# Kernel tuning notes

Measured on AMD Instinct MI355X. Metric: run time of the kernel, lower is better.

## Reference

```python
import jax, jax.numpy as jnp
import numpy as np

H = 16  # num_attention_heads
LN_EPS = 1e-12


def setup_inputs() -> dict:
    key = jax.random.key(0)
    ks = jax.random.split(key, 13)
    S, B, D = 2048, 2, 1024
    std = 0.02
    return {
        "query_tensor": jax.random.normal(ks[0], (S, B, D), jnp.float32),
        "key_tensor": jax.random.normal(ks[1], (S, B, D), jnp.float32),
        "value_tensor": jax.random.normal(ks[2], (S, B, D), jnp.float32),
        "Wq": jax.random.normal(ks[3], (D, D), jnp.float32) * std,
        "bq": jnp.zeros((D,), jnp.float32),
        "Wk": jax.random.normal(ks[4], (D, D), jnp.float32) * std,
        "bk": jnp.zeros((D,), jnp.float32),
        "Wv": jax.random.normal(ks[5], (D, D), jnp.float32) * std,
        "bv": jnp.zeros((D,), jnp.float32),
        "Wo": jax.random.normal(ks[6], (D, D), jnp.float32) * std,
        "bo": jnp.zeros((D,), jnp.float32),
        "ln_w": jnp.ones((D,), jnp.float32),
        "ln_b": jnp.zeros((D,), jnp.float32),
    }


def _layernorm(x, w, b):
    u = jnp.mean(x, axis=-1, keepdims=True)
    s = jnp.mean(jnp.square(x - u), axis=-1, keepdims=True)
    return w * ((x - u) / jnp.sqrt(s + LN_EPS)) + b


def reference(query_tensor, key_tensor, value_tensor, Wq, bq, Wk, bk, Wv, bv, Wo, bo, ln_w, ln_b):
    S, B, D = query_tensor.shape
    dh = D // H
    # QKV projections (nn.Linear: x @ W.T + b)
    q = query_tensor @ Wq.T + bq          # (S, B, D)
    k = key_tensor @ Wk.T + bk            # (Sk, B, D)
    v = value_tensor @ Wv.T + bv          # (Sk, B, D)
    # (S, B, D) -> (B*H, S, dh)
    q = q.reshape(S, B * H, dh).transpose(1, 0, 2)
    k = k.reshape(-1, B * H, dh).transpose(1, 0, 2)
    v = v.reshape(-1, B * H, dh).transpose(1, 0, 2)
    # NOTE: original code has NO 1/sqrt(dh) scaling
    scores = jnp.einsum('nqd,nkd->nqk', q, k)            # (B*H, S, Sk)
    probs = jax.nn.softmax(scores, axis=-1)
    # dropout is identity in eval mode
    ctx = jnp.einsum('nqk,nkd->nqd', probs, v)           # (B*H, S, dh)
    ctx = ctx.transpose(1, 0, 2).reshape(S, B, D)
    # BertSelfOutput: dense + residual + LayerNorm (dropout identity)
    out = ctx @ Wo.T + bo
    return _layernorm(out + query_tensor, ln_w, ln_b)
```

## Files before the change

### kernel.cpp

```cpp
#include <hip/hip_runtime.h>

#define SEQ    2048
#define BATCH  2
#define DMODEL 1024
#define NHEAD  16
#define DH     64
#define MROWS  (SEQ*BATCH)
#define RS     (BATCH*DMODEL)
#define LN_EPS 1e-12f
#define LOG2E  1.4426950408889634f

typedef __attribute__((ext_vector_type(8))) short short8;
typedef __attribute__((ext_vector_type(4))) float floatx4;

#define AS_GLOBAL __attribute__((address_space(1)))
#define AS_LDS    __attribute__((address_space(3)))

__device__ __forceinline__ float bf2f(unsigned short s) {
    union { unsigned u; float f; } a; a.u = ((unsigned)s) << 16; return a.f;
}
__device__ __forceinline__ unsigned short f2bf(float x) {
    union { float f; unsigned u; } a; a.f = x;
    unsigned r = a.u + 0x7fffu + ((a.u >> 16) & 1u);
    return (unsigned short)(r >> 16);
}
__device__ __forceinline__ unsigned cvt_pk_bf16(float a, float b) {
    unsigned r;
    asm("v_cvt_pk_bf16_f32 %0, %1, %2" : "=v"(r) : "v"(a), "v"(b));
    return r;
}
__device__ __forceinline__ float max3f(float a, float b, float c) {
    float r;
    asm("v_max3_f32 %0, %1, %2, %3" : "=v"(r) : "v"(a), "v"(b), "v"(c));
    return r;
}
__device__ __forceinline__ float fast_exp2(float x) {
#if __has_builtin(__builtin_amdgcn_exp2f)
    return __builtin_amdgcn_exp2f(x);
#else
    return exp2f(x);
#endif
}
__device__ __forceinline__ uint4 cvt8(const float* __restrict__ p) {
    float4 x0 = *(const float4*)(p);
    float4 x1 = *(const float4*)(p + 4);
    union { uint4 u; unsigned short s[8]; } r;
    r.s[0] = f2bf(x0.x); r.s[1] = f2bf(x0.y);
    r.s[2] = f2bf(x0.z); r.s[3] = f2bf(x0.w);
    r.s[4] = f2bf(x1.x); r.s[5] = f2bf(x1.y);
    r.s[6] = f2bf(x1.z); r.s[7] = f2bf(x1.w);
    return r.u;
}
__device__ __forceinline__ uint4 cvt8s(const float* __restrict__ p, float sc) {
    float4 x0 = *(const float4*)(p);
    float4 x1 = *(const float4*)(p + 4);
    union { uint4 u; unsigned short s[8]; } r;
    r.s[0] = f2bf(x0.x*sc); r.s[1] = f2bf(x0.y*sc);
    r.s[2] = f2bf(x0.z*sc); r.s[3] = f2bf(x0.w*sc);
    r.s[4] = f2bf(x1.x*sc); r.s[5] = f2bf(x1.y*sc);
    r.s[6] = f2bf(x1.z*sc); r.s[7] = f2bf(x1.w*sc);
    return r.u;
}

__global__ void beacon_kernel(float* out, float val) {
    if (threadIdx.x == 0) out[0] = val;
}

__global__ __launch_bounds__(256)
void cvt_kernel(const float* __restrict__ s0, const float* __restrict__ s1,
                const float* __restrict__ s2, const float* __restrict__ s3,
                const float* __restrict__ s4, const float* __restrict__ s5,
                const float* __restrict__ s6,
                unsigned short* __restrict__ d0, unsigned short* __restrict__ d1,
                unsigned short* __restrict__ d2, unsigned short* __restrict__ d3,
                unsigned short* __restrict__ d4, unsigned short* __restrict__ d5,
                unsigned short* __restrict__ d6)
{
    const float* srcs[7] = {s0, s1, s2, s3, s4, s5, s6};
    unsigned short* dsts[7] = {d0, d1, d2, d3, d4, d5, d6};
    const int cnts[7] = {4194304, 4194304, 4194304, 1048576, 1048576, 1048576, 1048576};
    const float scl[7] = {1.f, 1.f, 1.f, LOG2E, 1.f, 1.f, 1.f};
    const int z = blockIdx.z;
    const float* src = srcs[z];
    unsigned short* dst = dsts[z];
    const int count = cnts[z];
    const float sc = scl[z];
    const int stride = gridDim.x * 256 * 8;
    for (int i = (blockIdx.x * 256 + threadIdx.x) * 8; i < count; i += stride)
        *(uint4*)&dst[i] = cvt8s(&src[i], sc);
}

__global__ __launch_bounds__(256)
void vt_kernel(const unsigned short* __restrict__ Vb,
               unsigned short* __restrict__ VT)
{
    __shared__ __align__(16) short T[64*72];
    const int tid = threadIdx.x;
    const int s0 = blockIdx.x * 64;
    const int bh = blockIdx.y;
    const int b = bh >> 4, h = bh & 15;

    #pragma unroll
    for (int rep = 0; rep < 2; ++rep) {
        int c = tid + rep * 256;
        int s = c >> 3, cc = c & 7;
        *(uint4*)&T[s*72 + cc*8] =
            *(const uint4*)&Vb[((s0 + s) * BATCH + b) * DMODEL + h*64 + cc*8];
    }
    __syncthreads();
    #pragma unroll
    for (int rep = 0; rep < 2; ++rep) {
        int o = tid + rep * 256;
        int d = o >> 3, sc = o & 7;
        union { uint4 u; unsigned short e[8]; } pk;
        #pragma unroll
        for (int j = 0; j < 8; ++j)
            pk.e[j] = (unsigned short)T[(sc*8 + j)*72 + d];
        *(uint4*)&VT[bh*(DH*SEQ) + d*SEQ + s0 + sc*8] = pk.u;
    }
}

template<int OUTF32>
__device__ __forceinline__ void gemm_bf16_body(
    const unsigned short* __restrict__ A,
    const unsigned short* __restrict__ W,
    const float* __restrict__ bias, float bscale,
    void* __restrict__ Cout)
{
    __shared__ __align__(16) short Alds[2][128*32];
    __shared__ __align__(16) short Blds[2][128*32];

    const int tid  = threadIdx.x;
    const int lane = tid & 63;
    const int wave = tid >> 6;
    const int lrow = lane & 15;
    const int lq   = lane >> 4;
    const int m0 = blockIdx.x * 128;
    const int n0 = blockIdx.y * 128;
    const int mw = (wave >> 1) * 64;
    const int nw = (wave & 1) * 64;
    const int K  = DMODEL;

    const int chunk0 = tid;
    const int chunk1 = tid + 256;
    const int row0 = chunk0 >> 2, col0 = (chunk0 & 3) << 3;
    const int row1 = chunk1 >> 2, col1 = (chunk1 & 3) << 3;
    const unsigned short* gA0 = &A[(m0 + row0) * K + col0];
    const unsigned short* gA1 = &A[(m0 + row1) * K + col1];
    const unsigned short* gB0 = &W[(n0 + row0) * K + col0];
    const unsigned short* gB1 = &W[(n0 + row1) * K + col1];

    auto stage = [&](int k0, int b) {
        __builtin_amdgcn_global_load_lds((const AS_GLOBAL unsigned int*)(gA0 + k0),
            (AS_LDS unsigned int*)&Alds[b][(wave*64)*8], 16, 0, 0);
        __builtin_amdgcn_global_load_lds((const AS_GLOBAL unsigned int*)(gA1 + k0),
            (AS_LDS unsigned int*)&Alds[b][(256 + wave*64)*8], 16, 0, 0);
        __builtin_amdgcn_global_load_lds((const AS_GLOBAL unsigned int*)(gB0 + k0),
            (AS_LDS unsigned int*)&Blds[b][(wave*64)*8], 16, 0, 0);
        __builtin_amdgcn_global_load_lds((const AS_GLOBAL unsigned int*)(gB1 + k0),
            (AS_LDS unsigned int*)&Blds[b][(256 + wave*64)*8], 16, 0, 0);
    };

    floatx4 zero = {0.f, 0.f, 0.f, 0.f};
    floatx4 acc[4][4];
    #pragma unroll
    for (int i = 0; i < 4; ++i)
        #pragma unroll
        for (int j = 0; j < 4; ++j) acc[i][j] = zero;

    stage(0, 0);
    __syncthreads();

    for (int k0 = 0; k0 < K; k0 += 32) {
        const int cur = (k0 >> 5) & 1;
        if (k0 + 32 < K) stage(k0 + 32, cur ^ 1);
        short8 af[4], bfg[4];
        #pragma unroll
        for (int mi = 0; mi < 4; ++mi)
            af[mi] = *(const short8*)&Alds[cur][(mw + mi*16 + lrow)*32 + lq*8];
        #pragma unroll
        for (int ni = 0; ni < 4; ++ni)
            bfg[ni] = *(const short8*)&Blds[cur][(nw + ni*16 + lrow)*32 + lq*8];
        #pragma unroll
        for (int mi = 0; mi < 4; ++mi)
            #pragma unroll
            for (int ni = 0; ni < 4; ++ni)
                acc[mi][ni] = __builtin_amdgcn_mfma_f32_16x16x32_bf16(af[mi], bfg[ni], acc[mi][ni], 0, 0, 0);
        __syncthreads();
    }

    #pragma unroll
    for (int mi = 0; mi < 4; ++mi) {
        #pragma unroll
        for (int ni = 0; ni < 4; ++ni) {
            int n = n0 + nw + ni*16 + lrow;
            float bv_ = bias[n] * bscale;
            #pragma unroll
            for (int r = 0; r < 4; ++r) {
                int m = m0 + mw + mi*16 + lq*4 + r;
                float v = acc[mi][ni][r] + bv_;
                if (OUTF32) ((float*)Cout)[m * DMODEL + n] = v;
                else ((unsigned short*)Cout)[m * DMODEL + n] = f2bf(v);
            }
        }
    }
}

__global__ __launch_bounds__(256)
void qkv_bf16(const unsigned short* __restrict__ qb, const unsigned short* __restrict__ kb,
              const unsigned short* __restrict__ vb,
              const unsigned short* __restrict__ Wqb, const float* __restrict__ bq,
              const unsigned short* __restrict__ Wkb, const float* __restrict__ bk,
              const unsigned short* __restrict__ Wvb, const float* __restrict__ bv,
              unsigned short* __restrict__ Qo, unsigned short* __restrict__ Ko,
              unsigned short* __restrict__ Vo)
{
    const unsigned short *A, *W; const float* B; unsigned short* C; float bs;
    if (blockIdx.z == 0)      { A = qb; W = Wqb; B = bq; C = Qo; bs = LOG2E; }
    else if (blockIdx.z == 1) { A = kb; W = Wkb; B = bk; C = Ko; bs = 1.f; }
    else                      { A = vb; W = Wvb; B = bv; C = Vo; bs = 1.f; }
    gemm_bf16_body<0>(A, W, B, bs, C);
}

__global__ __launch_bounds__(256)
void oproj_bf16(const unsigned short* __restrict__ Cx,
                const unsigned short* __restrict__ Wob, const float* __restrict__ bo,
                float* __restrict__ O32)
{
    gemm_bf16_body<1>(Cx, Wob, bo, 1.f, O32);
}

__global__ __launch_bounds__(256)
void qkv_mfma(const float* __restrict__ q_in, const float* __restrict__ k_in,
              const float* __restrict__ v_in,
              const float* __restrict__ Wq, const float* __restrict__ bq,
              const float* __restrict__ Wk, const float* __restrict__ bk,
              const float* __restrict__ Wv, const float* __restrict__ bv,
              unsigned short* __restrict__ Qo, unsigned short* __restrict__ Ko,
              unsigned short* __restrict__ Vo)
{
    const float *A, *W, *B; unsigned short* C;
    if (blockIdx.z == 0)      { A = q_in; W = Wq; B = bq; C = Qo; }
    else if (blockIdx.z == 1) { A = k_in; W = Wk; B = bk; C = Ko; }
    else                      { A = v_in; W = Wv; B = bv; C = Vo; }

    __shared__ __align__(16) short Alds[128*32];
    __shared__ __align__(16) short Blds[128*32];
    const int tid  = threadIdx.x;
    const int lane = tid & 63;
    const int wave = tid >> 6;
    const int lrow = lane & 15;
    const int lq   = lane >> 4;
    const int m0 = blockIdx.x * 128;
    const int n0 = blockIdx.y * 128;
    const int mw = (wave >> 1) * 64;
    const int nw = (wave & 1) * 64;
    const int K  = DMODEL;

    floatx4 zero = {0.f, 0.f, 0.f, 0.f};
    floatx4 acc[4][4];
    #pragma unroll
    for (int i = 0; i < 4; ++i)
        #pragma unroll
        for (int j = 0; j < 4; ++j) acc[i][j] = zero;

    for (int k0 = 0; k0 < K; k0 += 32) {
        #pragma unroll
        for (int rep = 0; rep < 2; ++rep) {
            int chunk = tid + rep * 256;
            int row = chunk >> 2;
            int col = (chunk & 3) << 3;
            *(uint4*)&Alds[row*32 + col] = cvt8(&A[(m0 + row) * K + k0 + col]);
            *(uint4*)&Blds[row*32 + col] = cvt8(&W[(n0 + row) * K + k0 + col]);
        }
        __syncthreads();
        short8 af[4], bfg[4];
        #pragma unroll
        for (int mi = 0; mi < 4; ++mi)
            af[mi] = *(const short8*)&Alds[(mw + mi*16 + lrow)*32 + lq*8];
        #pragma unroll
        for (int ni = 0; ni < 4; ++ni)
            bfg[ni] = *(const short8*)&Blds[(nw + ni*16 + lrow)*32 + lq*8];
        #pragma unroll
        for (int mi = 0; mi < 4; ++mi)
            #pragma unroll
            for (int ni = 0; ni < 4; ++ni)
                acc[mi][ni] = __builtin_amdgcn_mfma_f32_16x16x32_bf16(af[mi], bfg[ni], acc[mi][ni], 0, 0, 0);
        __syncthreads();
    }

    #pragma unroll
    for (int mi = 0; mi < 4; ++mi) {
        #pragma unroll
        for (int ni = 0; ni < 4; ++ni) {
            int n = n0 + nw + ni*16 + lrow;
            float bv_ = B[n];
            #pragma unroll
            for (int r = 0; r < 4; ++r) {
                int m = m0 + mw + mi*16 + lq*4 + r;
                C[m * DMODEL + n] = f2bf(acc[mi][ni][r] + bv_);
            }
        }
    }
}

__global__ __launch_bounds__(256)
void oproj_mfma(const unsigned short* __restrict__ Cx,
                const float* __restrict__ Wo, const float* __restrict__ bo,
                float* __restrict__ O32)
{
    __shared__ __align__(16) short Alds[128*32];
    __shared__ __align__(16) short Blds[128*32];
    const int tid  = threadIdx.x;
    const int lane = tid & 63;
    const int wave = tid >> 6;
    const int lrow = lane & 15;
    const int lq   = lane >> 4;
    const int m0 = blockIdx.x * 128;
    const int n0 = blockIdx.y * 128;
    const int mw = (wave >> 1) * 64;
    const int nw = (wave & 1) * 64;
    const int K  = DMODEL;

    floatx4 zero = {0.f, 0.f, 0.f, 0.f};
    floatx4 acc[4][4];
    #pragma unroll
    for (int i = 0; i < 4; ++i)
        #pragma unroll
        for (int j = 0; j < 4; ++j) acc[i][j] = zero;

    for (int k0 = 0; k0 < K; k0 += 32) {
        #pragma unroll
        for (int rep = 0; rep < 2; ++rep) {
            int chunk = tid + rep * 256;
            int row = chunk >> 2;
            int col = (chunk & 3) << 3;
            *(uint4*)&Alds[row*32 + col] = *(const uint4*)&Cx[(m0 + row) * K + k0 + col];
            *(uint4*)&Blds[row*32 + col] = cvt8(&Wo[(n0 + row) * K + k0 + col]);
        }
        __syncthreads();
        short8 af[4], bfg[4];
        #pragma unroll
        for (int mi = 0; mi < 4; ++mi)
            af[mi] = *(const short8*)&Alds[(mw + mi*16 + lrow)*32 + lq*8];
        #pragma unroll
        for (int ni = 0; ni < 4; ++ni)
            bfg[ni] = *(const short8*)&Blds[(nw + ni*16 + lrow)*32 + lq*8];
        #pragma unroll
        for (int mi = 0; mi < 4; ++mi)
            #pragma unroll
            for (int ni = 0; ni < 4; ++ni)
                acc[mi][ni] = __builtin_amdgcn_mfma_f32_16x16x32_bf16(af[mi], bfg[ni], acc[mi][ni], 0, 0, 0);
        __syncthreads();
    }

    #pragma unroll
    for (int mi = 0; mi < 4; ++mi) {
        #pragma unroll
        for (int ni = 0; ni < 4; ++ni) {
            int n = n0 + nw + ni*16 + lrow;
            float bv_ = bo[n];
            #pragma unroll
            for (int r = 0; r < 4; ++r) {
                int m = m0 + mw + mi*16 + lq*4 + r;
                O32[m * DMODEL + n] = acc[mi][ni][r] + bv_;
            }
        }
    }
}

__global__ __launch_bounds__(256)
void attn_mfma5(const unsigned short* __restrict__ Q,
                const unsigned short* __restrict__ Kg,
                const unsigned short* __restrict__ VT,
                unsigned short* __restrict__ Ctx)
{
    __shared__ __align__(16) short SMEM[20480];

    const int tid  = threadIdx.x;
    const int lane = tid & 63;
    const int wave = tid >> 6;
    const int lrow = lane & 15;
    const int lq   = lane >> 4;

    const int q0 = blockIdx.x * 64;
    const int bh = blockIdx.y;
    const int off = (bh >> 4) * DMODEL + (bh & 15) * DH;
    const unsigned short* VTb = VT + bh * (DH * SEQ);
    short* const psw = &SMEM[16384 + wave * 1024];

    auto stageKV = [&](int kt, int b) {
        const int kbase = kt * 64;
        short* ksb = &SMEM[b * 8192];
        short* vtb = &SMEM[b * 8192 + 4096];
        #pragma unroll
        for (int rep = 0; rep < 2; ++rep) {
            int c = rep*256 + tid;
            int r = c >> 3, cc = c & 7;
            int sw = ((cc ^ (r & 7)) << 3);
            __builtin_amdgcn_global_load_lds(
                (const AS_GLOBAL unsigned int*)&Kg[(kbase + r) * RS + off + sw],
                (AS_LDS unsigned int*)&ksb[(rep*256 + wave*64) * 8], 16, 0, 0);
            __builtin_amdgcn_global_load_lds(
                (const AS_GLOBAL unsigned int*)&VTb[r * SEQ + kbase + sw],
                (AS_LDS unsigned int*)&vtb[(rep*256 + wave*64) * 8], 16, 0, 0);
        }
    };

    stageKV(0, 0);

    const int qrow = q0 + wave*16 + lrow;
    short8 qf[2];
    qf[0] = *(const short8*)&Q[qrow * RS + off + lq*8];
    qf[1] = *(const short8*)&Q[qrow * RS + off + 32 + lq*8];

    floatx4 zero = {0.f, 0.f, 0.f, 0.f};
    float m_i = 0.f, l_i = 0.f;
    floatx4 oacc[4];
    #pragma unroll
    for (int ni = 0; ni < 4; ++ni) oacc[ni] = zero;

    __syncthreads();

    for (int kt = 0; kt < SEQ/64; ++kt) {
        const int cur = kt & 1;
        if (kt + 1 < SEQ/64) stageKV(kt + 1, cur ^ 1);
        const short* ksb = &SMEM[cur * 8192];
        const short* vtb = &SMEM[cur * 8192 + 4096];

        floatx4 sacc[4];
        const float negm = -m_i;
        floatx4 minit = {negm, negm, negm, negm};
        #pragma unroll
        for (int ni = 0; ni < 4; ++ni) sacc[ni] = minit;
        __builtin_amdgcn_s_setprio(1);
        #pragma unroll
        for (int ni = 0; ni < 4; ++ni) {
            #pragma unroll
            for (int kk = 0; kk < 2; ++kk) {
                int key = ni*16 + lrow;
                int cc  = kk*4 + lq;
                short8 kf = *(const short8*)&ksb[key*64 + ((cc ^ (key & 7)) << 3)];
                sacc[ni] = __builtin_amdgcn_mfma_f32_16x16x32_bf16(kf, qf[kk], sacc[ni], 0, 0, 0);
            }
        }
        __builtin_amdgcn_s_setprio(0);

        float a0 = max3f(sacc[0][0], sacc[0][1], sacc[0][2]);
        float a1 = max3f(sacc[0][3], sacc[1][0], sacc[1][1]);
        float a2 = max3f(sacc[1][2], sacc[1][3], sacc[2][0]);
        float a3 = max3f(sacc[2][1], sacc[2][2], sacc[2][3]);
        float a4 = max3f(sacc[3][0], sacc[3][1], sacc[3][2]);
        float b0 = max3f(a0, a1, a2);
        float b1 = max3f(a3, a4, sacc[3][3]);
        float mx = fmaxf(b0, b1);
        mx = fmaxf(mx, __shfl_xor(mx, 16));
        mx = fmaxf(mx, __shfl_xor(mx, 32));

        float p[4][4];
        if (__all(mx <= 8.f)) {
            #pragma unroll
            for (int ni = 0; ni < 4; ++ni)
                #pragma unroll
                for (int r = 0; r < 4; ++r)
                    p[ni][r] = fast_exp2(sacc[ni][r]);
        } else {
            float shift = fmaxf(mx, 0.f);
            float alpha = fast_exp2(-shift);
            l_i *= alpha;
            #pragma unroll
            for (int ni = 0; ni < 4; ++ni)
                #pragma unroll
                for (int r = 0; r < 4; ++r) oacc[ni][r] *= alpha;
            m_i += shift;
            #pragma unroll
            for (int ni = 0; ni < 4; ++ni)
                #pragma unroll
                for (int r = 0; r < 4; ++r)
                    p[ni][r] = fast_exp2(sacc[ni][r] - shift);
        }

        float s00 = (p[0][0] + p[0][1]) + (p[0][2] + p[0][3]);
        float s01 = (p[1][0] + p[1][1]) + (p[1][2] + p[1][3]);
        float s10 = (p[2][0] + p[2][1]) + (p[2][2] + p[2][3]);
        float s11 = (p[3][0] + p[3][1]) + (p[3][2] + p[3][3]);
        float psum = (s00 + s01) + (s10 + s11);
        psum += __shfl_xor(psum, 16);
        psum += __shfl_xor(psum, 32);
        l_i += psum;

        #pragma unroll
        for (int ni = 0; ni < 4; ++ni) {
            uint2 pk;
            pk.x = cvt_pk_bf16(p[ni][0], p[ni][1]);
            pk.y = cvt_pk_bf16(p[ni][2], p[ni][3]);
            int t  = ni*2 + (lq >> 1);
            int tp = t ^ (lrow & 7);
            *(uint2*)&psw[lrow*64 + tp*8 + (lq & 1)*4] = pk;
        }
        __builtin_amdgcn_wave_barrier();

        short8 pf[2];
        #pragma unroll
        for (int kk = 0; kk < 2; ++kk) {
            int t  = kk*4 + lq;
            int tp = t ^ (lrow & 7);
            pf[kk] = *(const short8*)&psw[lrow*64 + tp*8];
        }

        __builtin_amdgcn_s_setprio(1);
        #pragma unroll
        for (int ni = 0; ni < 4; ++ni) {
            #pragma unroll
            for (int kk = 0; kk < 2; ++kk) {
                int d  = ni*16 + lrow;
                int cc = kk*4 + lq;
                short8 vf = *(const short8*)&vtb[d*64 + ((cc ^ (d & 7)) << 3)];
                oacc[ni] = __builtin_amdgcn_mfma_f32_16x16x32_bf16(vf, pf[kk], oacc[ni], 0, 0, 0);
            }
        }
        __builtin_amdgcn_s_setprio(0);

        __syncthreads();
    }

    const float inv = 1.f / l_i;
    #pragma unroll
    for (int ni = 0; ni < 4; ++ni) {
        uint2 ok;
        ok.x = cvt_pk_bf16(oacc[ni][0] * inv, oacc[ni][1] * inv);
        ok.y = cvt_pk_bf16(oacc[ni][2] * inv, oacc[ni][3] * inv);
        *(uint2*)&Ctx[qrow * RS + off + ni*16 + lq*4] = ok;
    }
}

__global__ __launch_bounds__(256)
void attn_mfma2(const unsigned short* __restrict__ Q,
                const unsigned short* __restrict__ Kg,
                const unsigned short* __restrict__ V,
                unsigned short* __restrict__ Ctx)
{
    __shared__ __align__(16) short Qs[64*72];
    __shared__ __align__(16) short Ks[64*72];
    __shared__ __align__(16) short Vt[64*72];
    __shared__ __align__(16) short Ps[4][16*72];

    const int tid  = threadIdx.x;
    const int lane = tid & 63;
    const int wave = tid >> 6;
    const int lrow = lane & 15;
    const int lq   = lane >> 4;

    const int q0 = blockIdx.x * 64;
    const int bh = blockIdx.y;
    const int off = (bh >> 4) * DMODEL + (bh & 15) * DH;

    #pragma unroll
    for (int rep = 0; rep < 2; ++rep) {
        int chunk = tid + rep * 256;
        int r = chunk >> 3;
        int c = (chunk & 7) << 3;
        *(uint4*)&Qs[r*72 + c] = *(const uint4*)&Q[(q0 + r) * RS + off + c];
    }
    __syncthreads();

    short8 qf[2];
    #pragma unroll
    for (int ks = 0; ks < 2; ++ks)
        qf[ks] = *(const short8*)&Qs[(wave*16 + lrow)*72 + ks*32 + lq*8];

    floatx4 zero = {0.f, 0.f, 0.f, 0.f};
    float m_i = -1e30f, l_i = 0.f;
    floatx4 oacc[4];
    #pragma unroll
    for (int ni = 0; ni < 4; ++ni) oacc[ni] = zero;

    for (int kt = 0; kt < SEQ/64; ++kt) {
        __syncthreads();
        const int kbase = kt * 64;
        #pragma unroll
        for (int rep = 0; rep < 2; ++rep) {
            int chunk = tid + rep * 256;
            int r = chunk >> 3;
            int c = (chunk & 7) << 3;
            *(uint4*)&Ks[r*72 + c] = *(const uint4*)&Kg[(kbase + r) * RS + off + c];
            uint4 vv = *(const uint4*)&V[(kbase + r) * RS + off + c];
            union { uint4 u; short s[8]; } uv; uv.u = vv;
            int swz = (chunk & 7) << 3;
            #pragma unroll
            for (int j = 0; j < 8; ++j)
                Vt[(c + j)*72 + (r ^ swz)] = uv.s[j];
        }
        __syncthreads();

        floatx4 sacc[4];
        #pragma unroll
        for (int ni = 0; ni < 4; ++ni) sacc[ni] = zero;
        #pragma unroll
        for (int ni = 0; ni < 4; ++ni) {
            #pragma unroll
            for (int ks = 0; ks < 2; ++ks) {
                short8 kf = *(const short8*)&Ks[(ni*16 + lrow)*72 + ks*32 + lq*8];
                sacc[ni] = __builtin_amdgcn_mfma_f32_16x16x32_bf16(kf, qf[ks], sacc[ni], 0, 0, 0);
            }
        }

        float mx = sacc[0][0];
        #pragma unroll
        for (int ni = 0; ni < 4; ++ni)
            #pragma unroll
            for (int r = 0; r < 4; ++r) mx = fmaxf(mx, sacc[ni][r]);
        mx = fmaxf(mx, __shfl_xor(mx, 16));
        mx = fmaxf(mx, __shfl_xor(mx, 32));
        float mnew = fmaxf(m_i, mx);
        float alpha = __expf(m_i - mnew);
        float p[4][4];
        float psum = 0.f;
        #pragma unroll
        for (int ni = 0; ni < 4; ++ni)
            #pragma unroll
            for (int r = 0; r < 4; ++r) {
                p[ni][r] = __expf(sacc[ni][r] - mnew);
                psum += p[ni][r];
            }
        psum += __shfl_xor(psum, 16);
        psum += __shfl_xor(psum, 32);
        l_i = l_i * alpha + psum;
        m_i = mnew;
        #pragma unroll
        for (int ni = 0; ni < 4; ++ni)
            #pragma unroll
            for (int r = 0; r < 4; ++r) oacc[ni][r] *= alpha;

        #pragma unroll
        for (int ni = 0; ni < 4; ++ni) {
            uint2 pk;
            pk.x = (unsigned)f2bf(p[ni][0]) | ((unsigned)f2bf(p[ni][1]) << 16);
            pk.y = (unsigned)f2bf(p[ni][2]) | ((unsigned)f2bf(p[ni][3]) << 16);
            *(uint2*)&Ps[wave][lrow*72 + ni*16 + lq*4] = pk;
        }
        __builtin_amdgcn_wave_barrier();

        short8 pf[2];
        #pragma unroll
        for (int ks = 0; ks < 2; ++ks)
            pf[ks] = *(const short8*)&Ps[wave][lrow*72 + ks*32 + lq*8];
        #pragma unroll
        for (int ni = 0; ni < 4; ++ni) {
            #pragma unroll
            for (int ks = 0; ks < 2; ++ks) {
                int d  = ni*16 + lrow;
                int kk = ks*32 + lq*8;
                int swz = ((d >> 3) & 7) << 3;
                short8 vf = *(const short8*)&Vt[d*72 + (kk ^ swz)];
                oacc[ni] = __builtin_amdgcn_mfma_f32_16x16x32_bf16(vf, pf[ks], oacc[ni], 0, 0, 0);
            }
        }
    }

    const float inv = 1.f / l_i;
    const int q = q0 + wave*16 + lrow;
    #pragma unroll
    for (int ni = 0; ni < 4; ++ni) {
        uint2 ok;
        ok.x = (unsigned)f2bf(oacc[ni][0] * inv) | ((unsigned)f2bf(oacc[ni][1] * inv) << 16);
        ok.y = (unsigned)f2bf(oacc[ni][2] * inv) | ((unsigned)f2bf(oacc[ni][3] * inv) << 16);
        *(uint2*)&Ctx[q * RS + off + ni*16 + lq*4] = ok;
    }
}

__global__ __launch_bounds__(256)
void ln2_kernel(const float* __restrict__ O,
                const float* __restrict__ resid,
                const float* __restrict__ w,
                const float* __restrict__ bb,
                float* __restrict__ out)
{
    __shared__ float r1s[4];
    __shared__ float r2s[4];
    const int row = blockIdx.x;
    const int tid = threadIdx.x;
    const int c4 = tid * 4;

    float4 o4 = *(const float4*)&O[row * DMODEL + c4];
    float4 q4 = *(const float4*)&resid[row * DMODEL + c4];
    float x0 = o4.x + q4.x;
    float x1 = o4.y + q4.y;
    float x2 = o4.z + q4.z;
    float x3 = o4.w + q4.w;

    float s1 = x0 + x1 + x2 + x3;
    float s2 = x0*x0 + x1*x1 + x2*x2 + x3*x3;
    #pragma unroll
    for (int o = 32; o > 0; o >>= 1) {
        s1 += __shfl_xor(s1, o);
        s2 += __shfl_xor(s2, o);
    }
    if ((tid & 63) == 0) { r1s[tid >> 6] = s1; r2s[tid >> 6] = s2; }
    __syncthreads();
    float t1 = r1s[0] + r1s[1] + r1s[2] + r1s[3];
    float t2 = r2s[0] + r2s[1] + r2s[2] + r2s[3];

    const float mean = t1 * (1.f / DMODEL);
    float var = t2 * (1.f / DMODEL) - mean * mean;
    var = fmaxf(var, 0.f);
    const float rstd = rsqrtf(var + LN_EPS);

    float4 w4 = *(const float4*)&w[c4];
    float4 b4 = *(const float4*)&bb[c4];
    float4 y;
    y.x = w4.x * ((x0 - mean) * rstd) + b4.x;
    y.y = w4.y * ((x1 - mean) * rstd) + b4.y;
    y.z = w4.z * ((x2 - mean) * rstd) + b4.z;
    y.w = w4.w * ((x3 - mean) * rstd) + b4.w;
    *(float4*)&out[row * DMODEL + c4] = y;
}

extern "C" void kernel_launch(void* const* d_in, const int* in_sizes, int n_in,
                              void* d_out, int out_size, void* d_ws, size_t ws_size,
                              hipStream_t stream) {
    const float* q_in = (const float*)d_in[0];
    const float* k_in = (const float*)d_in[1];
    const float* v_in = (const float*)d_in[2];
    const float* Wq = (const float*)d_in[3];  const float* bq = (const float*)d_in[4];
    const float* Wk = (const float*)d_in[5];  const float* bk = (const float*)d_in[6];
    const float* Wv = (const float*)d_in[7];  const float* bv = (const float*)d_in[8];
    const float* Wo = (const float*)d_in[9];  const float* bo = (const float*)d_in[10];
    const float* lnw = (const float*)d_in[11]; const float* lnb = (const float*)d_in[12];

    char* wsb = (char*)d_ws;
    unsigned short* QCtx = (unsigned short*)d_out;
    float*          outF = (float*)d_out;
    dim3 blk(256);

    if (ws_size >= (48u << 20)) {
        unsigned short* qb  = (unsigned short*)(wsb);
        unsigned short* kb  = (unsigned short*)(wsb + (8u  << 20));
        unsigned short* vb  = (unsigned short*)(wsb + (16u << 20));
        unsigned short* Wqb = (unsigned short*)(wsb + (24u << 20));
        unsigned short* Wkb = (unsigned short*)(wsb + (26u << 20));
        unsigned short* Wvb = (unsigned short*)(wsb + (28u << 20));
        unsigned short* Wob = (unsigned short*)(wsb + (30u << 20));
        unsigned short* Kb  = (unsigned short*)(wsb + (32u << 20));
        unsigned short* Vb  = (unsigned short*)(wsb + (40u << 20));
        unsigned short* VT  = (unsigned short*)(wsb);
        float*          O32 = (float*)(wsb);

        cvt_kernel<<<dim3(512, 1, 7), blk, 0, stream>>>(
            q_in, k_in, v_in, Wq, Wk, Wv, Wo,
            qb, kb, vb, Wqb, Wkb, Wvb, Wob);
        qkv_bf16<<<dim3(MROWS/128, DMODEL/128, 3), blk, 0, stream>>>(
            qb, kb, vb, Wqb, bq, Wkb, bk, Wvb, bv, QCtx, Kb, Vb);
        vt_kernel<<<dim3(SEQ/64, BATCH*NHEAD), blk, 0, stream>>>(Vb, VT);
        attn_mfma5<<<dim3(SEQ/64, BATCH*NHEAD), blk, 0, stream>>>(QCtx, Kb, VT, QCtx);
        oproj_bf16<<<dim3(MROWS/128, DMODEL/128), blk, 0, stream>>>(QCtx, Wob, bo, O32);
        ln2_kernel<<<dim3(MROWS), blk, 0, stream>>>(O32, q_in, lnw, lnb, outF);
    } else if (ws_size >= (16u << 20)) {
        unsigned short* Kb  = (unsigned short*)(wsb);
        unsigned short* Vb  = (unsigned short*)(wsb + (8u << 20));
        float*          O32 = (float*)(wsb);
        qkv_mfma<<<dim3(MROWS/128, DMODEL/128, 3), blk, 0, stream>>>(
            q_in, k_in, v_in, Wq, bq, Wk, bk, Wv, bv, QCtx, Kb, Vb);
        attn_mfma2<<<dim3(SEQ/64, BATCH*NHEAD), blk, 0, stream>>>(QCtx, Kb, Vb, QCtx);
        oproj_mfma<<<dim3(MROWS/128, DMODEL/128), blk, 0, stream>>>(QCtx, Wo, bo, O32);
        ln2_kernel<<<dim3(MROWS), blk, 0, stream>>>(O32, q_in, lnw, lnb, outF);
    } else {
        beacon_kernel<<<1, 64, 0, stream>>>((float*)d_out, 300.0f);
    }
}
```

Baseline: 259.1 us.

## Remap block IDs for XCD-local L2 reuse and use true running-max softmax

Flattens the grids of the QKV, attention and output-projection kernels and remaps block indices so that blocks sharing the same weights, or the same head's K/V, land on the same XCD (round-robin over 8). The goal is better per-XCD L2 reuse. The attention kernel also replaces the fixed zero-based max with a proper running max initialised to -1e30, rescaling only when the max rises by more than 8. This makes the softmax robust to large unscaled scores, at the cost of a subtract per exponent instead of folding the shift into the accumulator init.

```diff
diff --git a/kernel.cpp b/kernel.cpp
--- a/kernel.cpp
+++ b/kernel.cpp
@@ -125,7 +125,7 @@
     const unsigned short* __restrict__ A,
     const unsigned short* __restrict__ W,
     const float* __restrict__ bias, float bscale,
-    void* __restrict__ Cout)
+    void* __restrict__ Cout, int m0, int n0)
 {
     __shared__ __align__(16) short Alds[2][128*32];
     __shared__ __align__(16) short Blds[2][128*32];
@@ -135,8 +135,6 @@
     const int wave = tid >> 6;
     const int lrow = lane & 15;
     const int lq   = lane >> 4;
-    const int m0 = blockIdx.x * 128;
-    const int n0 = blockIdx.y * 128;
     const int mw = (wave >> 1) * 64;
     const int nw = (wave & 1) * 64;
     const int K  = DMODEL;
@@ -215,11 +213,18 @@
               unsigned short* __restrict__ Qo, unsigned short* __restrict__ Ko,
               unsigned short* __restrict__ Vo)
 {
+    const int flat = blockIdx.x;
+    const int ns = (flat & 7) * 96 + (flat >> 3);
+    const int z  = ns >> 8;
+    const int r  = ns & 255;
+    const int n0 = (r & 7) * 128;
+    const int m0 = (r >> 3) * 128;
+
     const unsigned short *A, *W; const float* B; unsigned short* C; float bs;
-    if (blockIdx.z == 0)      { A = qb; W = Wqb; B = bq; C = Qo; bs = LOG2E; }
-    else if (blockIdx.z == 1) { A = kb; W = Wkb; B = bk; C = Ko; bs = 1.f; }
-    else                      { A = vb; W = Wvb; B = bv; C = Vo; bs = 1.f; }
-    gemm_bf16_body<0>(A, W, B, bs, C);
+    if (z == 0)      { A = qb; W = Wqb; B = bq; C = Qo; bs = LOG2E; }
+    else if (z == 1) { A = kb; W = Wkb; B = bk; C = Ko; bs = 1.f; }
+    else             { A = vb; W = Wvb; B = bv; C = Vo; bs = 1.f; }
+    gemm_bf16_body<0>(A, W, B, bs, C, m0, n0);
 }
 
 __global__ __launch_bounds__(256)
@@ -227,7 +232,11 @@
                 const unsigned short* __restrict__ Wob, const float* __restrict__ bo,
                 float* __restrict__ O32)
 {
-    gemm_bf16_body<1>(Cx, Wob, bo, 1.f, O32);
+    const int flat = blockIdx.x;
+    const int ns = (flat & 7) * 32 + (flat >> 3);
+    const int n0 = (ns & 7) * 128;
+    const int m0 = (ns >> 3) * 128;
+    gemm_bf16_body<1>(Cx, Wob, bo, 1.f, O32, m0, n0);
 }
 
 __global__ __launch_bounds__(256)
@@ -370,7 +379,7 @@
 }
 
 __global__ __launch_bounds__(256)
-void attn_mfma5(const unsigned short* __restrict__ Q,
+void attn_mfma6(const unsigned short* __restrict__ Q,
                 const unsigned short* __restrict__ Kg,
                 const unsigned short* __restrict__ VT,
                 unsigned short* __restrict__ Ctx)
@@ -383,8 +392,11 @@
     const int lrow = lane & 15;
     const int lq   = lane >> 4;
 
-    const int q0 = blockIdx.x * 64;
-    const int bh = blockIdx.y;
+    const int flat = blockIdx.x + (blockIdx.y << 5);
+    const int ns   = (flat & 7) * 128 + (flat >> 3);
+    const int q0 = (ns & 31) * 64;
+    const int bh = ns >> 5;
+
     const int off = (bh >> 4) * DMODEL + (bh & 15) * DH;
     const unsigned short* VTb = VT + bh * (DH * SEQ);
     short* const psw = &SMEM[16384 + wave * 1024];
@@ -415,7 +427,7 @@
     qf[1] = *(const short8*)&Q[qrow * RS + off + 32 + lq*8];
 
     floatx4 zero = {0.f, 0.f, 0.f, 0.f};
-    float m_i = 0.f, l_i = 0.f;
+    float m_i = -1e30f, l_i = 0.f;
     floatx4 oacc[4];
     #pragma unroll
     for (int ni = 0; ni < 4; ++ni) oacc[ni] = zero;
@@ -429,10 +441,8 @@
         const short* vtb = &SMEM[cur * 8192 + 4096];
 
         floatx4 sacc[4];
-        const float negm = -m_i;
-        floatx4 minit = {negm, negm, negm, negm};
-        #pragma unroll
-        for (int ni = 0; ni < 4; ++ni) sacc[ni] = minit;
+        #pragma unroll
+        for (int ni = 0; ni < 4; ++ni) sacc[ni] = zero;
         __builtin_amdgcn_s_setprio(1);
         #pragma unroll
         for (int ni = 0; ni < 4; ++ni) {
@@ -457,28 +467,22 @@
         mx = fmaxf(mx, __shfl_xor(mx, 16));
         mx = fmaxf(mx, __shfl_xor(mx, 32));
 
-        float p[4][4];
-        if (__all(mx <= 8.f)) {
-            #pragma unroll
-            for (int ni = 0; ni < 4; ++ni)
-                #pragma unroll
-                for (int r = 0; r < 4; ++r)
-                    p[ni][r] = fast_exp2(sacc[ni][r]);
-        } else {
-            float shift = fmaxf(mx, 0.f);
-            float alpha = fast_exp2(-shift);
+        if (!__all(mx <= m_i + 8.f)) {
+            float mnew = fmaxf(m_i, mx);
+            float alpha = fast_exp2(m_i - mnew);
             l_i *= alpha;
             #pragma unroll
             for (int ni = 0; ni < 4; ++ni)
                 #pragma unroll
                 for (int r = 0; r < 4; ++r) oacc[ni][r] *= alpha;
-            m_i += shift;
-            #pragma unroll
-            for (int ni = 0; ni < 4; ++ni)
-                #pragma unroll
-                for (int r = 0; r < 4; ++r)
-                    p[ni][r] = fast_exp2(sacc[ni][r] - shift);
-        }
+            m_i = mnew;
+        }
+        float p[4][4];
+        #pragma unroll
+        for (int ni = 0; ni < 4; ++ni)
+            #pragma unroll
+            for (int r = 0; r < 4; ++r)
+                p[ni][r] = fast_exp2(sacc[ni][r] - m_i);
 
         float s00 = (p[0][0] + p[0][1]) + (p[0][2] + p[0][3]);
         float s01 = (p[1][0] + p[1][1]) + (p[1][2] + p[1][3]);
@@ -749,11 +753,11 @@
         cvt_kernel<<<dim3(512, 1, 7), blk, 0, stream>>>(
             q_in, k_in, v_in, Wq, Wk, Wv, Wo,
             qb, kb, vb, Wqb, Wkb, Wvb, Wob);
-        qkv_bf16<<<dim3(MROWS/128, DMODEL/128, 3), blk, 0, stream>>>(
+        qkv_bf16<<<dim3(768), blk, 0, stream>>>(
             qb, kb, vb, Wqb, bq, Wkb, bk, Wvb, bv, QCtx, Kb, Vb);
         vt_kernel<<<dim3(SEQ/64, BATCH*NHEAD), blk, 0, stream>>>(Vb, VT);
-        attn_mfma5<<<dim3(SEQ/64, BATCH*NHEAD), blk, 0, stream>>>(QCtx, Kb, VT, QCtx);
-        oproj_bf16<<<dim3(MROWS/128, DMODEL/128), blk, 0, stream>>>(QCtx, Wob, bo, O32);
+        attn_mfma6<<<dim3(SEQ/64, BATCH*NHEAD), blk, 0, stream>>>(QCtx, Kb, VT, QCtx);
+        oproj_bf16<<<dim3(256), blk, 0, stream>>>(QCtx, Wob, bo, O32);
         ln2_kernel<<<dim3(MROWS), blk, 0, stream>>>(O32, q_in, lnw, lnb, outF);
     } else if (ws_size >= (16u << 20)) {
         unsigned short* Kb  = (unsigned short*)(wsb);
```

Result: faster. 250.2 us (-3.4%).
